# Performance work log

Hardware: AMD Instinct MI355X
Metric: run time of the kernel (lower is better)

## Reference

```python
import jax, jax.numpy as jnp
import numpy as np

N = 100000
IN_CH, HID_CH, OUT_CH = 128, 128, 64
E = 1600000


def gcn_layer(x, W, b, src, dst, num_nodes):
    """PyG GCNConv: add self-loops, symmetric deg^-1/2 normalization,
    x' = D^-1/2 (A+I) D^-1/2 (x W) + b."""
    # degrees including self-loops (deg = 1 + in-degree with unit edge weights)
    ones = jnp.ones(dst.shape[0], dtype=x.dtype)
    deg = jnp.ones(num_nodes, dtype=x.dtype).at[dst].add(ones)
    dinv = jax.lax.rsqrt(deg)
    h = x @ W  # [N, out_dim] -- transform before propagate (PyG order)
    # neighbor messages
    norm = dinv[src] * dinv[dst]                      # [E]
    msg = h[src] * norm[:, None]                      # [E, out_dim] (traffic-bound)
    agg = jax.ops.segment_sum(msg, dst, num_segments=num_nodes)
    # self-loop contribution: norm_ii = dinv[i]^2
    agg = agg + h * (dinv * dinv)[:, None]
    return agg + b


def setup_inputs() -> dict:
    key = jax.random.key(0)
    ks = jax.random.split(key, 7)
    x = jax.random.normal(ks[0], (N, IN_CH), dtype=jnp.float32)
    edge_index = jax.random.randint(ks[1], (2, E), 0, N, dtype=jnp.int64)
    # Glorot-style init like PyG GCNConv
    W1 = jax.random.normal(ks[2], (IN_CH, HID_CH), dtype=jnp.float32) * (1.0 / np.sqrt(IN_CH))
    b1 = jnp.zeros((HID_CH,), dtype=jnp.float32)
    W2 = jax.random.normal(ks[3], (HID_CH, OUT_CH), dtype=jnp.float32) * (1.0 / np.sqrt(HID_CH))
    b2 = jnp.zeros((OUT_CH,), dtype=jnp.float32)
    return {"x": x, "edge_index": edge_index, "W1": W1, "b1": b1, "W2": W2, "b2": b2}


def reference(x, edge_index, W1, b1, W2, b2):
    src, dst = edge_index[0], edge_index[1]
    h = gcn_layer(x, W1, b1, src, dst, N)
    h = jax.nn.relu(h)  # dropout is identity in eval mode
    out = gcn_layer(h, W2, b2, src, dst, N)
    return out
```

## Files before the change

kernel.cpp:

```cpp
#include <hip/hip_runtime.h>
#include <hip/hip_fp16.h>

#define NNODES 100000
#define NEDGES 1600000
#define IN_C   128
#define HID_C  128
#define OUT_C  64

#define CAP     64
#define OVF_MAX 4096

#define BUCKET_SHIFT 7
#define BUCKET_NODES 128
#define NB ((NNODES + BUCKET_NODES - 1) / BUCKET_NODES)
#define BCAP 3072
#define BCNT_STRIDE 16
#define EB 4096
#define NBLK_A ((NEDGES + EB - 1) / EB)
#define GB ((NNODES + 63) / 64)

typedef __attribute__((ext_vector_type(8))) _Float16 half8;
typedef __attribute__((ext_vector_type(4))) _Float16 half4;
typedef __attribute__((ext_vector_type(4))) float floatx4;

__device__ __forceinline__ long long load_idx(const void* p, long long i, int is64) {
  return is64 ? ((const long long*)p)[i] : (long long)((const int*)p)[i];
}

__global__ void prep_kernel(const void* eidx, int* flag, int* bcnt,
                            int* ovf_cnt, int* ovfA_cnt,
                            const float* __restrict__ W1,
                            const float* __restrict__ W2,
                            _Float16* __restrict__ Wt1,
                            _Float16* __restrict__ Wt2) {
  int i = blockIdx.x * 256 + threadIdx.x;
  if (i < NB * BCNT_STRIDE) bcnt[i] = 0;
  if (i == 0) { *ovf_cnt = 0; *ovfA_cnt = 0; }
  if (blockIdx.x == 0 && threadIdx.x < 64) {
    const unsigned* w = (const unsigned*)eidx;
    unsigned v = w[2 * threadIdx.x + 1];
    unsigned long long bad = __ballot(v != 0u);
    if (threadIdx.x == 0) *flag = (bad == 0ull) ? 1 : 0;
  }
  const int stride = gridDim.x * 256;
  for (int t = i; t < IN_C * HID_C; t += stride) {
    int n = t >> 7, k = t & 127;
    Wt1[t] = (_Float16)W1[k * HID_C + n];
  }
  for (int t = i; t < HID_C * OUT_C; t += stride) {
    int n = t >> 7, k = t & 127;
    Wt2[t] = (_Float16)W2[k * OUT_C + n];
  }
}

__global__ __launch_bounds__(512) void binA_kernel(const void* __restrict__ eidx,
                                                   const int* __restrict__ flag,
                                                   int* __restrict__ bcnt,
                                                   unsigned* __restrict__ buf,
                                                   int* __restrict__ ovfA_cnt,
                                                   int2* __restrict__ ovfA) {
  __shared__ unsigned se[EB];
  __shared__ unsigned short be[EB];
  __shared__ int hist[NB];
  __shared__ int base[NB];
  __shared__ int ofs[NB];
  const int tid = threadIdx.x;
  const int e0 = blockIdx.x * EB;
  const int e1 = min(e0 + EB, NEDGES);
  const int m = e1 - e0;
  const int is64 = *flag;

  for (int b = tid; b < NB; b += 512) { hist[b] = 0; ofs[b] = 0; }
  __syncthreads();

  for (int k = tid; k < m; k += 512) {
    int e = e0 + k;
    int s = (int)load_idx(eidx, e, is64);
    int d = (int)load_idx(eidx, (long long)NEDGES + e, is64);
    int b = d >> BUCKET_SHIFT;
    se[k] = (unsigned)s | ((unsigned)(d & (BUCKET_NODES - 1)) << 17);
    be[k] = (unsigned short)b;
    atomicAdd(&hist[b], 1);
  }
  __syncthreads();

  int rot = (blockIdx.x * 131) % NB;
  for (int idx = tid; idx < NB; idx += 512) {
    int b = idx + rot;
    if (b >= NB) b -= NB;
    int h = hist[b];
    if (h > 0) base[b] = atomicAdd(&bcnt[b * BCNT_STRIDE], h);
  }
  __syncthreads();

  for (int k = tid; k < m; k += 512) {
    unsigned u = se[k];
    int b = be[k];
    int ko = atomicAdd(&ofs[b], 1);
    int slot = base[b] + ko;
    if (slot < BCAP) {
      buf[(size_t)b * BCAP + slot] = u;
    } else {
      int p = atomicAdd(ovfA_cnt, 1);
      if (p < OVF_MAX)
        ovfA[p] = make_int2((int)(u & 0x1FFFFu),
                            (b << BUCKET_SHIFT) | (int)(u >> 17));
    }
  }
}

__global__ __launch_bounds__(512) void binB_kernel(const int* __restrict__ bcnt,
                                                   const unsigned* __restrict__ buf,
                                                   const int* __restrict__ ovfA_cnt,
                                                   const int2* __restrict__ ovfA,
                                                   int* __restrict__ cnt,
                                                   float* __restrict__ dinv,
                                                   int* __restrict__ pad_csr,
                                                   int* __restrict__ ovf_cnt,
                                                   int2* __restrict__ ovf) {
  __shared__ int pad[BUCKET_NODES * CAP];
  __shared__ int lcnt[BUCKET_NODES];
  const int b = blockIdx.x;
  const int tid = threadIdx.x;
  const int node0 = b << BUCKET_SHIFT;

  if (tid < BUCKET_NODES) lcnt[tid] = 0;
  __syncthreads();

  const int n = min(bcnt[b * BCNT_STRIDE], BCAP);
  for (int k = tid; k < n; k += 512) {
    unsigned u = buf[(size_t)b * BCAP + k];
    int s = (int)(u & 0x1FFFFu);
    int dl = (int)(u >> 17);
    int slot = atomicAdd(&lcnt[dl], 1);
    if (slot < CAP) {
      pad[dl * CAP + slot] = s;
    } else {
      int p = atomicAdd(ovf_cnt, 1);
      if (p < OVF_MAX) ovf[p] = make_int2(s, node0 + dl);
    }
  }
  int na = min(*ovfA_cnt, OVF_MAX);
  for (int t = tid; t < na; t += 512) {
    int2 p = ovfA[t];
    if ((p.y >> BUCKET_SHIFT) == b) {
      int dl = p.y & (BUCKET_NODES - 1);
      int slot = atomicAdd(&lcnt[dl], 1);
      if (slot < CAP) {
        pad[dl * CAP + slot] = p.x;
      } else {
        int q = atomicAdd(ovf_cnt, 1);
        if (q < OVF_MAX) ovf[q] = make_int2(p.x, p.y);
      }
    }
  }
  __syncthreads();

  constexpr int I4PN = CAP / 4;
  for (int q = tid; q < BUCKET_NODES * I4PN; q += 512) {
    int dl = q / I4PN;
    int gn = node0 + dl;
    if (gn < NNODES) {
      int c = (q % I4PN) * 4;
      *(int4*)&pad_csr[(size_t)gn * CAP + c] = *(const int4*)&pad[dl * CAP + c];
    }
  }
  if (tid < BUCKET_NODES && node0 + tid < NNODES) {
    int c = lcnt[tid];
    cnt[node0 + tid] = c;
    dinv[node0 + tid] = rsqrtf((float)(c + 1));
  }
}

__global__ __launch_bounds__(256) void gemm1_kernel(const float* __restrict__ x,
                                                    const _Float16* __restrict__ Wt1,
                                                    const float* __restrict__ dinv,
                                                    _Float16* __restrict__ h1s) {
  constexpr int K = IN_C, N = HID_C, KP = K + 8;
  __shared__ alignas(16) _Float16 Alds[64 * KP];
  __shared__ alignas(16) _Float16 Wlds[N * KP];
  const int tid = threadIdx.x;
  const int row0 = blockIdx.x * 64;

  for (int idx = tid; idx < N * (K / 8); idx += 256) {
    int n = idx >> 4, k16 = idx & 15;
    *(int4*)&Wlds[n * KP + k16 * 8] = *(const int4*)&Wt1[n * K + k16 * 8];
  }
  constexpr int F4PR = K / 4;
  for (int idx = tid; idx < 64 * F4PR; idx += 256) {
    int lr = idx >> 5;
    int c4 = (idx & 31) * 4;
    int gr = row0 + lr;
    if (gr > NNODES - 1) gr = NNODES - 1;
    float4 v = *(const float4*)&x[(size_t)gr * K + c4];
    half4 h = {(_Float16)v.x, (_Float16)v.y, (_Float16)v.z, (_Float16)v.w};
    *(half4*)&Alds[lr * KP + c4] = h;
  }
  __syncthreads();

  const int w = tid >> 6;
  const int lane = tid & 63;
  const int g = lane >> 4;
  const int mi = lane & 15;
  constexpr int NT = N / 16;
  floatx4 acc[NT];
#pragma unroll
  for (int t = 0; t < NT; ++t) acc[t] = (floatx4){0.f, 0.f, 0.f, 0.f};
  const _Float16* arow = &Alds[(w * 16 + mi) * KP];
#pragma unroll
  for (int ks = 0; ks < K / 32; ++ks) {
    half8 a = *(const half8*)(arow + ks * 32 + g * 8);
#pragma unroll
    for (int t = 0; t < NT; ++t) {
      half8 b = *(const half8*)&Wlds[(t * 16 + mi) * KP + ks * 32 + g * 8];
      acc[t] = __builtin_amdgcn_mfma_f32_16x16x32_f16(a, b, acc[t], 0, 0, 0);
    }
  }
#pragma unroll
  for (int r = 0; r < 4; ++r) {
    int grow = row0 + w * 16 + 4 * g + r;
    if (grow < NNODES) {
      float s = dinv[grow];
      _Float16* orow = h1s + (size_t)grow * N + mi;
#pragma unroll
      for (int t = 0; t < NT; ++t) orow[t * 16] = (_Float16)(acc[t][r] * s);
    }
  }
}

__global__ __launch_bounds__(256) void gemm2_kernel(const _Float16* __restrict__ hid,
                                                    const _Float16* __restrict__ Wt2,
                                                    const float* __restrict__ dinv,
                                                    _Float16* __restrict__ h2s) {
  constexpr int K = HID_C, N = OUT_C, KP = K + 8;
  __shared__ alignas(16) _Float16 Alds[64 * KP];
  __shared__ alignas(16) _Float16 Wlds[N * KP];
  const int tid = threadIdx.x;
  const int row0 = blockIdx.x * 64;

  for (int idx = tid; idx < N * (K / 8); idx += 256) {
    int n = idx >> 4, k16 = idx & 15;
    *(int4*)&Wlds[n * KP + k16 * 8] = *(const int4*)&Wt2[n * K + k16 * 8];
  }
  for (int idx = tid; idx < 64 * (K / 8); idx += 256) {
    int lr = idx >> 4, k16 = idx & 15;
    int gr = row0 + lr;
    if (gr > NNODES - 1) gr = NNODES - 1;
    *(int4*)&Alds[lr * KP + k16 * 8] =
        *(const int4*)&hid[(size_t)gr * K + k16 * 8];
  }
  __syncthreads();

  const int w = tid >> 6;
  const int lane = tid & 63;
  const int g = lane >> 4;
  const int mi = lane & 15;
  constexpr int NT = N / 16;
  floatx4 acc[NT];
#pragma unroll
  for (int t = 0; t < NT; ++t) acc[t] = (floatx4){0.f, 0.f, 0.f, 0.f};
  const _Float16* arow = &Alds[(w * 16 + mi) * KP];
#pragma unroll
  for (int ks = 0; ks < K / 32; ++ks) {
    half8 a = *(const half8*)(arow + ks * 32 + g * 8);
#pragma unroll
    for (int t = 0; t < NT; ++t) {
      half8 b = *(const half8*)&Wlds[(t * 16 + mi) * KP + ks * 32 + g * 8];
      acc[t] = __builtin_amdgcn_mfma_f32_16x16x32_f16(a, b, acc[t], 0, 0, 0);
    }
  }
#pragma unroll
  for (int r = 0; r < 4; ++r) {
    int grow = row0 + w * 16 + 4 * g + r;
    if (grow < NNODES) {
      float s = dinv[grow];
      _Float16* orow = h2s + (size_t)grow * N + mi;
#pragma unroll
      for (int t = 0; t < NT; ++t) orow[t * 16] = (_Float16)(acc[t][r] * s);
    }
  }
}

struct F8 {
  float x0, x1, x2, x3, x4, x5, x6, x7;
};

__device__ __forceinline__ void add_h8(F8& a, const __half* p) {
  int4 r = *(const int4*)p;
  const __half2* h = (const __half2*)&r;
  float2 f0 = __half22float2(h[0]);
  float2 f1 = __half22float2(h[1]);
  float2 f2 = __half22float2(h[2]);
  float2 f3 = __half22float2(h[3]);
  a.x0 += f0.x; a.x1 += f0.y; a.x2 += f1.x; a.x3 += f1.y;
  a.x4 += f2.x; a.x5 += f2.y; a.x6 += f3.x; a.x7 += f3.y;
}

__global__ __launch_bounds__(256) void gather1_kernel(
    const int* __restrict__ cnt, const int* __restrict__ pad_csr,
    const float* __restrict__ dinv, const __half* __restrict__ Hs1,
    const float* __restrict__ b1, const int* __restrict__ ovf_cnt,
    const int2* __restrict__ ovf, _Float16* __restrict__ hidden) {
  constexpr int C = HID_C;
  const int half = blockIdx.x & 1;
  const int tile = blockIdx.x >> 1;
  const int il = threadIdx.x >> 2;
  const int c16 = half * 64 + (threadIdx.x & 3) * 16;
  const int i = tile * 64 + il;
  if (i >= NNODES) return;

  const float di = dinv[i];
  const int deg = cnt[i];
  const int beg = i * CAP;
  const int end = beg + min(deg, CAP);
  const int* __restrict__ lst = pad_csr;
  const __half* __restrict__ Hb = Hs1 + c16;

  F8 a0l = {}, a0h = {}, a1l = {}, a1h = {};
  {
    const __half* p = Hb + (size_t)i * C;
    add_h8(a0l, p);
    add_h8(a0h, p + 8);
  }
  int j = beg;
  for (; j + 8 <= end; j += 8) {
    int4 sa = *(const int4*)&lst[j];
    int4 sb = *(const int4*)&lst[j + 4];
    const __half* p0 = Hb + (size_t)sa.x * C;
    const __half* p1 = Hb + (size_t)sa.y * C;
    const __half* p2 = Hb + (size_t)sa.z * C;
    const __half* p3 = Hb + (size_t)sa.w * C;
    add_h8(a0l, p0); add_h8(a0h, p0 + 8);
    add_h8(a1l, p1); add_h8(a1h, p1 + 8);
    add_h8(a0l, p2); add_h8(a0h, p2 + 8);
    add_h8(a1l, p3); add_h8(a1h, p3 + 8);
    const __half* p4 = Hb + (size_t)sb.x * C;
    const __half* p5 = Hb + (size_t)sb.y * C;
    const __half* p6 = Hb + (size_t)sb.z * C;
    const __half* p7 = Hb + (size_t)sb.w * C;
    add_h8(a0l, p4); add_h8(a0h, p4 + 8);
    add_h8(a1l, p5); add_h8(a1h, p5 + 8);
    add_h8(a0l, p6); add_h8(a0h, p6 + 8);
    add_h8(a1l, p7); add_h8(a1h, p7 + 8);
  }
  for (; j + 2 <= end; j += 2) {
    const __half* p0 = Hb + (size_t)lst[j] * C;
    const __half* p1 = Hb + (size_t)lst[j + 1] * C;
    add_h8(a0l, p0); add_h8(a0h, p0 + 8);
    add_h8(a1l, p1); add_h8(a1h, p1 + 8);
  }
  if (j < end) {
    const __half* p0 = Hb + (size_t)lst[j] * C;
    add_h8(a0l, p0); add_h8(a0h, p0 + 8);
  }
  if (deg > CAP) {
    int nv = min(*ovf_cnt, OVF_MAX);
    for (int t = 0; t < nv; ++t) {
      int2 p = ovf[t];
      if (p.y == i) {
        const __half* q = Hb + (size_t)p.x * C;
        add_h8(a0l, q); add_h8(a0h, q + 8);
      }
    }
  }

  float4 bb0 = *(const float4*)&b1[c16];
  float4 bb1 = *(const float4*)&b1[c16 + 4];
  float4 bb2 = *(const float4*)&b1[c16 + 8];
  float4 bb3 = *(const float4*)&b1[c16 + 12];
  float o0 = fmaf(a0l.x0 + a1l.x0, di, bb0.x);
  float o1 = fmaf(a0l.x1 + a1l.x1, di, bb0.y);
  float o2 = fmaf(a0l.x2 + a1l.x2, di, bb0.z);
  float o3 = fmaf(a0l.x3 + a1l.x3, di, bb0.w);
  float o4 = fmaf(a0l.x4 + a1l.x4, di, bb1.x);
  float o5 = fmaf(a0l.x5 + a1l.x5, di, bb1.y);
  float o6 = fmaf(a0l.x6 + a1l.x6, di, bb1.z);
  float o7 = fmaf(a0l.x7 + a1l.x7, di, bb1.w);
  float o8 = fmaf(a0h.x0 + a1h.x0, di, bb2.x);
  float o9 = fmaf(a0h.x1 + a1h.x1, di, bb2.y);
  float o10 = fmaf(a0h.x2 + a1h.x2, di, bb2.z);
  float o11 = fmaf(a0h.x3 + a1h.x3, di, bb2.w);
  float o12 = fmaf(a0h.x4 + a1h.x4, di, bb3.x);
  float o13 = fmaf(a0h.x5 + a1h.x5, di, bb3.y);
  float o14 = fmaf(a0h.x6 + a1h.x6, di, bb3.z);
  float o15 = fmaf(a0h.x7 + a1h.x7, di, bb3.w);
  o0 = o0 > 0.f ? o0 : 0.f;   o1 = o1 > 0.f ? o1 : 0.f;
  o2 = o2 > 0.f ? o2 : 0.f;   o3 = o3 > 0.f ? o3 : 0.f;
  o4 = o4 > 0.f ? o4 : 0.f;   o5 = o5 > 0.f ? o5 : 0.f;
  o6 = o6 > 0.f ? o6 : 0.f;   o7 = o7 > 0.f ? o7 : 0.f;
  o8 = o8 > 0.f ? o8 : 0.f;   o9 = o9 > 0.f ? o9 : 0.f;
  o10 = o10 > 0.f ? o10 : 0.f; o11 = o11 > 0.f ? o11 : 0.f;
  o12 = o12 > 0.f ? o12 : 0.f; o13 = o13 > 0.f ? o13 : 0.f;
  o14 = o14 > 0.f ? o14 : 0.f; o15 = o15 > 0.f ? o15 : 0.f;

  _Float16* Out = hidden + (size_t)i * C + c16;
  half8 hv0 = {(_Float16)o0, (_Float16)o1, (_Float16)o2, (_Float16)o3,
               (_Float16)o4, (_Float16)o5, (_Float16)o6, (_Float16)o7};
  half8 hv1 = {(_Float16)o8, (_Float16)o9, (_Float16)o10, (_Float16)o11,
               (_Float16)o12, (_Float16)o13, (_Float16)o14, (_Float16)o15};
  *(half8*)Out = hv0;
  *(half8*)(Out + 8) = hv1;
}

__global__ __launch_bounds__(256) void gather2_kernel(
    const int* __restrict__ cnt, const int* __restrict__ pad_csr,
    const float* __restrict__ dinv, const __half* __restrict__ Hs2,
    const float* __restrict__ b2, const int* __restrict__ ovf_cnt,
    const int2* __restrict__ ovf, float* __restrict__ Out) {
  constexpr int C = OUT_C;
  const int half = blockIdx.x & 1;
  const int tile = blockIdx.x >> 1;
  const int il = threadIdx.x >> 1;
  const int c16 = half * 32 + (threadIdx.x & 1) * 16;
  const int i = tile * 128 + il;
  if (i >= NNODES) return;

  const float di = dinv[i];
  const int deg = cnt[i];
  const int beg = i * CAP;
  const int end = beg + min(deg, CAP);
  const int* __restrict__ lst = pad_csr;
  const __half* __restrict__ Hb = Hs2 + c16;

  F8 a0l = {}, a0h = {}, a1l = {}, a1h = {};
  {
    const __half* p = Hb + (size_t)i * C;
    add_h8(a0l, p);
    add_h8(a0h, p + 8);
  }
  int j = beg;
  for (; j + 8 <= end; j += 8) {
    int4 sa = *(const int4*)&lst[j];
    int4 sb = *(const int4*)&lst[j + 4];
    const __half* p0 = Hb + (size_t)sa.x * C;
    const __half* p1 = Hb + (size_t)sa.y * C;
    const __half* p2 = Hb + (size_t)sa.z * C;
    const __half* p3 = Hb + (size_t)sa.w * C;
    add_h8(a0l, p0); add_h8(a0h, p0 + 8);
    add_h8(a1l, p1); add_h8(a1h, p1 + 8);
    add_h8(a0l, p2); add_h8(a0h, p2 + 8);
    add_h8(a1l, p3); add_h8(a1h, p3 + 8);
    const __half* p4 = Hb + (size_t)sb.x * C;
    const __half* p5 = Hb + (size_t)sb.y * C;
    const __half* p6 = Hb + (size_t)sb.z * C;
    const __half* p7 = Hb + (size_t)sb.w * C;
    add_h8(a0l, p4); add_h8(a0h, p4 + 8);
    add_h8(a1l, p5); add_h8(a1h, p5 + 8);
    add_h8(a0l, p6); add_h8(a0h, p6 + 8);
    add_h8(a1l, p7); add_h8(a1h, p7 + 8);
  }
  for (; j + 2 <= end; j += 2) {
    const __half* p0 = Hb + (size_t)lst[j] * C;
    const __half* p1 = Hb + (size_t)lst[j + 1] * C;
    add_h8(a0l, p0); add_h8(a0h, p0 + 8);
    add_h8(a1l, p1); add_h8(a1h, p1 + 8);
  }
  if (j < end) {
    const __half* p0 = Hb + (size_t)lst[j] * C;
    add_h8(a0l, p0); add_h8(a0h, p0 + 8);
  }
  if (deg > CAP) {
    int nv = min(*ovf_cnt, OVF_MAX);
    for (int t = 0; t < nv; ++t) {
      int2 p = ovf[t];
      if (p.y == i) {
        const __half* q = Hb + (size_t)p.x * C;
        add_h8(a0l, q); add_h8(a0h, q + 8);
      }
    }
  }

  float4 bb0 = *(const float4*)&b2[c16];
  float4 bb1 = *(const float4*)&b2[c16 + 4];
  float4 bb2 = *(const float4*)&b2[c16 + 8];
  float4 bb3 = *(const float4*)&b2[c16 + 12];
  float* O = Out + (size_t)i * C + c16;
  *(float4*)O = make_float4(fmaf(a0l.x0 + a1l.x0, di, bb0.x),
                            fmaf(a0l.x1 + a1l.x1, di, bb0.y),
                            fmaf(a0l.x2 + a1l.x2, di, bb0.z),
                            fmaf(a0l.x3 + a1l.x3, di, bb0.w));
  *(float4*)(O + 4) = make_float4(fmaf(a0l.x4 + a1l.x4, di, bb1.x),
                                  fmaf(a0l.x5 + a1l.x5, di, bb1.y),
                                  fmaf(a0l.x6 + a1l.x6, di, bb1.z),
                                  fmaf(a0l.x7 + a1l.x7, di, bb1.w));
  *(float4*)(O + 8) = make_float4(fmaf(a0h.x0 + a1h.x0, di, bb2.x),
                                  fmaf(a0h.x1 + a1h.x1, di, bb2.y),
                                  fmaf(a0h.x2 + a1h.x2, di, bb2.z),
                                  fmaf(a0h.x3 + a1h.x3, di, bb2.w));
  *(float4*)(O + 12) = make_float4(fmaf(a0h.x4 + a1h.x4, di, bb3.x),
                                   fmaf(a0h.x5 + a1h.x5, di, bb3.y),
                                   fmaf(a0h.x6 + a1h.x6, di, bb3.z),
                                   fmaf(a0h.x7 + a1h.x7, di, bb3.w));
}

extern "C" void kernel_launch(void* const* d_in, const int* in_sizes, int n_in,
                              void* d_out, int out_size, void* d_ws, size_t ws_size,
                              hipStream_t stream) {
  const float* x = (const float*)d_in[0];
  const void* eidx = d_in[1];
  const float* W1 = (const float*)d_in[2];
  const float* b1 = (const float*)d_in[3];
  const float* W2 = (const float*)d_in[4];
  const float* b2 = (const float*)d_in[5];
  float* out = (float*)d_out;
  char* ws = (char*)d_ws;

  int*      flag     = (int*)(ws + 0);
  int*      ovf_cnt  = (int*)(ws + 512);
  int*      ovfA_cnt = (int*)(ws + 1024);
  int*      bcnt     = (int*)(ws + 1536);
  int*      cnt      = (int*)(ws + 52224);
  float*    dinv     = (float*)(ws + 452608);
  int2*     ovf      = (int2*)(ws + 852992);
  int2*     ovfA     = (int2*)(ws + 885760);
  _Float16* Wt1      = (_Float16*)(ws + 918528);
  _Float16* Wt2      = (_Float16*)(ws + 951296);
  unsigned* buf      = (unsigned*)(ws + 968192);
  int*      pad_csr  = (int*)(ws + 10577920);
  _Float16* h1s      = (_Float16*)(ws + 36178432);
  _Float16* hidden   = (_Float16*)(ws + 61778944);
  _Float16* h2s      = h1s;

  prep_kernel<<<(NB * BCNT_STRIDE + 255) / 256, 256, 0, stream>>>(
      eidx, flag, bcnt, ovf_cnt, ovfA_cnt, W1, W2, Wt1, Wt2);
  binA_kernel<<<NBLK_A, 512, 0, stream>>>(eidx, flag, bcnt, buf, ovfA_cnt, ovfA);
  binB_kernel<<<NB, 512, 0, stream>>>(bcnt, buf, ovfA_cnt, ovfA, cnt, dinv,
                                      pad_csr, ovf_cnt, ovf);
  gemm1_kernel<<<GB, 256, 0, stream>>>(x, Wt1, dinv, h1s);
  gather1_kernel<<<2 * GB, 256, 0, stream>>>(cnt, pad_csr, dinv,
                                             (const __half*)h1s, b1,
                                             ovf_cnt, ovf, hidden);
  gemm2_kernel<<<GB, 256, 0, stream>>>(hidden, Wt2, dinv, h2s);
  gather2_kernel<<<2 * ((NNODES + 127) / 128), 256, 0, stream>>>(
      cnt, pad_csr, dinv, (const __half*)h2s, b2, ovf_cnt, ovf, out);
}
```

Baseline: 293.0 us.

## Fuse edge binning with first GEMM, apply source norm in gather, halve CSR cap

The first GEMM is merged into the edge-binning kernel as extra blocks, so it no longer depends on degree normalisation. It now writes an unscaled h1 and overlaps with binning. The layer-1 gather multiplies each neighbour row by dinv[src] itself, which adds one scattered dinv load per edge. The padded CSR capacity drops from 64 to 32, which shrinks pad_csr traffic and workspace but relies on the overflow list for high-degree nodes. The gather index mapping is also simplified to a flat thread-per-16-channel layout.

```diff
diff --git a/kernel.cpp b/kernel.cpp
--- a/kernel.cpp
+++ b/kernel.cpp
@@ -7,7 +7,7 @@
 #define HID_C  128
 #define OUT_C  64
 
-#define CAP     64
+#define CAP     32
 #define OVF_MAX 4096
 
 #define BUCKET_SHIFT 7
@@ -53,58 +53,111 @@
   }
 }
 
-__global__ __launch_bounds__(512) void binA_kernel(const void* __restrict__ eidx,
-                                                   const int* __restrict__ flag,
-                                                   int* __restrict__ bcnt,
-                                                   unsigned* __restrict__ buf,
-                                                   int* __restrict__ ovfA_cnt,
-                                                   int2* __restrict__ ovfA) {
-  __shared__ unsigned se[EB];
-  __shared__ unsigned short be[EB];
-  __shared__ int hist[NB];
-  __shared__ int base[NB];
-  __shared__ int ofs[NB];
+__global__ __launch_bounds__(256) void binA_gemm1_kernel(
+    const void* __restrict__ eidx, const int* __restrict__ flag,
+    int* __restrict__ bcnt, unsigned* __restrict__ buf,
+    int* __restrict__ ovfA_cnt, int2* __restrict__ ovfA,
+    const float* __restrict__ x, const _Float16* __restrict__ Wt1,
+    _Float16* __restrict__ h1u) {
+  __shared__ alignas(16) char smem[52224];
   const int tid = threadIdx.x;
-  const int e0 = blockIdx.x * EB;
-  const int e1 = min(e0 + EB, NEDGES);
-  const int m = e1 - e0;
-  const int is64 = *flag;
-
-  for (int b = tid; b < NB; b += 512) { hist[b] = 0; ofs[b] = 0; }
-  __syncthreads();
-
-  for (int k = tid; k < m; k += 512) {
-    int e = e0 + k;
-    int s = (int)load_idx(eidx, e, is64);
-    int d = (int)load_idx(eidx, (long long)NEDGES + e, is64);
-    int b = d >> BUCKET_SHIFT;
-    se[k] = (unsigned)s | ((unsigned)(d & (BUCKET_NODES - 1)) << 17);
-    be[k] = (unsigned short)b;
-    atomicAdd(&hist[b], 1);
-  }
-  __syncthreads();
-
-  int rot = (blockIdx.x * 131) % NB;
-  for (int idx = tid; idx < NB; idx += 512) {
-    int b = idx + rot;
-    if (b >= NB) b -= NB;
-    int h = hist[b];
-    if (h > 0) base[b] = atomicAdd(&bcnt[b * BCNT_STRIDE], h);
-  }
-  __syncthreads();
-
-  for (int k = tid; k < m; k += 512) {
-    unsigned u = se[k];
-    int b = be[k];
-    int ko = atomicAdd(&ofs[b], 1);
-    int slot = base[b] + ko;
-    if (slot < BCAP) {
-      buf[(size_t)b * BCAP + slot] = u;
-    } else {
-      int p = atomicAdd(ovfA_cnt, 1);
-      if (p < OVF_MAX)
-        ovfA[p] = make_int2((int)(u & 0x1FFFFu),
-                            (b << BUCKET_SHIFT) | (int)(u >> 17));
+
+  if (blockIdx.x < NBLK_A) {
+    unsigned* se = (unsigned*)smem;
+    unsigned short* be = (unsigned short*)(smem + 16384);
+    int* hist = (int*)(smem + 24576);
+    int* base = (int*)(smem + 27712);
+    int* ofs  = (int*)(smem + 30848);
+    const int e0 = blockIdx.x * EB;
+    const int e1 = min(e0 + EB, NEDGES);
+    const int m = e1 - e0;
+    const int is64 = *flag;
+
+    for (int b = tid; b < NB; b += 256) { hist[b] = 0; ofs[b] = 0; }
+    __syncthreads();
+
+    for (int k = tid; k < m; k += 256) {
+      int e = e0 + k;
+      int s = (int)load_idx(eidx, e, is64);
+      int d = (int)load_idx(eidx, (long long)NEDGES + e, is64);
+      int b = d >> BUCKET_SHIFT;
+      se[k] = (unsigned)s | ((unsigned)(d & (BUCKET_NODES - 1)) << 17);
+      be[k] = (unsigned short)b;
+      atomicAdd(&hist[b], 1);
+    }
+    __syncthreads();
+
+    int rot = (blockIdx.x * 131) % NB;
+    for (int idx = tid; idx < NB; idx += 256) {
+      int b = idx + rot;
+      if (b >= NB) b -= NB;
+      int h = hist[b];
+      if (h > 0) base[b] = atomicAdd(&bcnt[b * BCNT_STRIDE], h);
+    }
+    __syncthreads();
+
+    for (int k = tid; k < m; k += 256) {
+      unsigned u = se[k];
+      int b = be[k];
+      int ko = atomicAdd(&ofs[b], 1);
+      int slot = base[b] + ko;
+      if (slot < BCAP) {
+        buf[(size_t)b * BCAP + slot] = u;
+      } else {
+        int p = atomicAdd(ovfA_cnt, 1);
+        if (p < OVF_MAX)
+          ovfA[p] = make_int2((int)(u & 0x1FFFFu),
+                              (b << BUCKET_SHIFT) | (int)(u >> 17));
+      }
+    }
+  } else {
+    constexpr int K = IN_C, N = HID_C, KP = K + 8;
+    _Float16* Alds = (_Float16*)smem;
+    _Float16* Wlds = (_Float16*)(smem + 17408);
+    const int row0 = (blockIdx.x - NBLK_A) * 64;
+
+    for (int idx = tid; idx < N * (K / 8); idx += 256) {
+      int n = idx >> 4, k16 = idx & 15;
+      *(int4*)&Wlds[n * KP + k16 * 8] = *(const int4*)&Wt1[n * K + k16 * 8];
+    }
+    constexpr int F4PR = K / 4;
+    for (int idx = tid; idx < 64 * F4PR; idx += 256) {
+      int lr = idx >> 5;
+      int c4 = (idx & 31) * 4;
+      int gr = row0 + lr;
+      if (gr > NNODES - 1) gr = NNODES - 1;
+      float4 v = *(const float4*)&x[(size_t)gr * K + c4];
+      half4 h = {(_Float16)v.x, (_Float16)v.y, (_Float16)v.z, (_Float16)v.w};
+      *(half4*)&Alds[lr * KP + c4] = h;
+    }
+    __syncthreads();
+
+    const int w = tid >> 6;
+    const int lane = tid & 63;
+    const int g = lane >> 4;
+    const int mi = lane & 15;
+    constexpr int NT = N / 16;
+    floatx4 acc[NT];
+#pragma unroll
+    for (int t = 0; t < NT; ++t) acc[t] = (floatx4){0.f, 0.f, 0.f, 0.f};
+    const _Float16* arow = &Alds[(w * 16 + mi) * KP];
+#pragma unroll
+    for (int ks = 0; ks < K / 32; ++ks) {
+      half8 a = *(const half8*)(arow + ks * 32 + g * 8);
+#pragma unroll
+      for (int t = 0; t < NT; ++t) {
+        half8 b = *(const half8*)&Wlds[(t * 16 + mi) * KP + ks * 32 + g * 8];
+        acc[t] = __builtin_amdgcn_mfma_f32_16x16x32_f16(a, b, acc[t], 0, 0, 0);
+      }
+    }
+#pragma unroll
+    for (int r = 0; r < 4; ++r) {
+      int grow = row0 + w * 16 + 4 * g + r;
+      if (grow < NNODES) {
+        _Float16* orow = h1u + (size_t)grow * N + mi;
+#pragma unroll
+        for (int t = 0; t < NT; ++t) orow[t * 16] = (_Float16)acc[t][r];
+      }
     }
   }
 }
@@ -172,60 +225,137 @@
   }
 }
 
-__global__ __launch_bounds__(256) void gemm1_kernel(const float* __restrict__ x,
-                                                    const _Float16* __restrict__ Wt1,
-                                                    const float* __restrict__ dinv,
-                                                    _Float16* __restrict__ h1s) {
-  constexpr int K = IN_C, N = HID_C, KP = K + 8;
-  __shared__ alignas(16) _Float16 Alds[64 * KP];
-  __shared__ alignas(16) _Float16 Wlds[N * KP];
-  const int tid = threadIdx.x;
-  const int row0 = blockIdx.x * 64;
-
-  for (int idx = tid; idx < N * (K / 8); idx += 256) {
-    int n = idx >> 4, k16 = idx & 15;
-    *(int4*)&Wlds[n * KP + k16 * 8] = *(const int4*)&Wt1[n * K + k16 * 8];
-  }
-  constexpr int F4PR = K / 4;
-  for (int idx = tid; idx < 64 * F4PR; idx += 256) {
-    int lr = idx >> 5;
-    int c4 = (idx & 31) * 4;
-    int gr = row0 + lr;
-    if (gr > NNODES - 1) gr = NNODES - 1;
-    float4 v = *(const float4*)&x[(size_t)gr * K + c4];
-    half4 h = {(_Float16)v.x, (_Float16)v.y, (_Float16)v.z, (_Float16)v.w};
-    *(half4*)&Alds[lr * KP + c4] = h;
-  }
-  __syncthreads();
-
-  const int w = tid >> 6;
-  const int lane = tid & 63;
-  const int g = lane >> 4;
-  const int mi = lane & 15;
-  constexpr int NT = N / 16;
-  floatx4 acc[NT];
-#pragma unroll
-  for (int t = 0; t < NT; ++t) acc[t] = (floatx4){0.f, 0.f, 0.f, 0.f};
-  const _Float16* arow = &Alds[(w * 16 + mi) * KP];
-#pragma unroll
-  for (int ks = 0; ks < K / 32; ++ks) {
-    half8 a = *(const half8*)(arow + ks * 32 + g * 8);
-#pragma unroll
-    for (int t = 0; t < NT; ++t) {
-      half8 b = *(const half8*)&Wlds[(t * 16 + mi) * KP + ks * 32 + g * 8];
-      acc[t] = __builtin_amdgcn_mfma_f32_16x16x32_f16(a, b, acc[t], 0, 0, 0);
-    }
-  }
-#pragma unroll
-  for (int r = 0; r < 4; ++r) {
-    int grow = row0 + w * 16 + 4 * g + r;
-    if (grow < NNODES) {
-      float s = dinv[grow];
-      _Float16* orow = h1s + (size_t)grow * N + mi;
-#pragma unroll
-      for (int t = 0; t < NT; ++t) orow[t * 16] = (_Float16)(acc[t][r] * s);
-    }
-  }
+struct F8 {
+  float x0, x1, x2, x3, x4, x5, x6, x7;
+};
+
+__device__ __forceinline__ void add_h8(F8& a, const __half* p) {
+  int4 r = *(const int4*)p;
+  const __half2* h = (const __half2*)&r;
+  float2 f0 = __half22float2(h[0]);
+  float2 f1 = __half22float2(h[1]);
+  float2 f2 = __half22float2(h[2]);
+  float2 f3 = __half22float2(h[3]);
+  a.x0 += f0.x; a.x1 += f0.y; a.x2 += f1.x; a.x3 += f1.y;
+  a.x4 += f2.x; a.x5 += f2.y; a.x6 += f3.x; a.x7 += f3.y;
+}
+
+__device__ __forceinline__ void add_h8s(F8& a, const __half* p, float s) {
+  int4 r = *(const int4*)p;
+  const __half2* h = (const __half2*)&r;
+  float2 f0 = __half22float2(h[0]);
+  float2 f1 = __half22float2(h[1]);
+  float2 f2 = __half22float2(h[2]);
+  float2 f3 = __half22float2(h[3]);
+  a.x0 = fmaf(s, f0.x, a.x0); a.x1 = fmaf(s, f0.y, a.x1);
+  a.x2 = fmaf(s, f1.x, a.x2); a.x3 = fmaf(s, f1.y, a.x3);
+  a.x4 = fmaf(s, f2.x, a.x4); a.x5 = fmaf(s, f2.y, a.x5);
+  a.x6 = fmaf(s, f3.x, a.x6); a.x7 = fmaf(s, f3.y, a.x7);
+}
+
+__global__ __launch_bounds__(256) void gather1d_kernel(
+    const int* __restrict__ cnt, const int* __restrict__ pad_csr,
+    const float* __restrict__ dinv, const __half* __restrict__ H,
+    const float* __restrict__ b1, const int* __restrict__ ovf_cnt,
+    const int2* __restrict__ ovf, _Float16* __restrict__ hidden) {
+  constexpr int C = HID_C;
+  constexpr int TPN = C / 16;
+  int gid = blockIdx.x * 256 + threadIdx.x;
+  int i = gid / TPN;
+  int c16 = (gid % TPN) * 16;
+  if (i >= NNODES) return;
+
+  const float di = dinv[i];
+  const int deg = cnt[i];
+  const int beg = i * CAP;
+  const int end = beg + min(deg, CAP);
+  const int* __restrict__ lst = pad_csr;
+  const __half* __restrict__ Hb = H + c16;
+
+  F8 a0l = {}, a0h = {}, a1l = {}, a1h = {};
+  {
+    const __half* p = Hb + (size_t)i * C;
+    add_h8s(a0l, p, di);
+    add_h8s(a0h, p + 8, di);
+  }
+  int j = beg;
+  for (; j + 8 <= end; j += 8) {
+    int4 sa = *(const int4*)&lst[j];
+    int4 sb = *(const int4*)&lst[j + 4];
+    float d0 = dinv[sa.x], d1 = dinv[sa.y], d2 = dinv[sa.z], d3 = dinv[sa.w];
+    float d4 = dinv[sb.x], d5 = dinv[sb.y], d6 = dinv[sb.z], d7 = dinv[sb.w];
+    const __half* p0 = Hb + (size_t)sa.x * C;
+    const __half* p1 = Hb + (size_t)sa.y * C;
+    const __half* p2 = Hb + (size_t)sa.z * C;
+    const __half* p3 = Hb + (size_t)sa.w * C;
+    add_h8s(a0l, p0, d0); add_h8s(a0h, p0 + 8, d0);
+    add_h8s(a1l, p1, d1); add_h8s(a1h, p1 + 8, d1);
+    add_h8s(a0l, p2, d2); add_h8s(a0h, p2 + 8, d2);
+    add_h8s(a1l, p3, d3); add_h8s(a1h, p3 + 8, d3);
+    const __half* p4 = Hb + (size_t)sb.x * C;
+    const __half* p5 = Hb + (size_t)sb.y * C;
+    const __half* p6 = Hb + (size_t)sb.z * C;
+    const __half* p7 = Hb + (size_t)sb.w * C;
+    add_h8s(a0l, p4, d4); add_h8s(a0h, p4 + 8, d4);
+    add_h8s(a1l, p5, d5); add_h8s(a1h, p5 + 8, d5);
+    add_h8s(a0l, p6, d6); add_h8s(a0h, p6 + 8, d6);
+    add_h8s(a1l, p7, d7); add_h8s(a1h, p7 + 8, d7);
+  }
+  for (; j < end; ++j) {
+    int s = lst[j];
+    float ds = dinv[s];
+    const __half* p0 = Hb + (size_t)s * C;
+    add_h8s(a0l, p0, ds); add_h8s(a0h, p0 + 8, ds);
+  }
+  if (deg > CAP) {
+    int nv = min(*ovf_cnt, OVF_MAX);
+    for (int t = 0; t < nv; ++t) {
+      int2 p = ovf[t];
+      if (p.y == i) {
+        float ds = dinv[p.x];
+        const __half* q = Hb + (size_t)p.x * C;
+        add_h8s(a0l, q, ds); add_h8s(a0h, q + 8, ds);
+      }
+    }
+  }
+
+  float s0 = a0l.x0 + a1l.x0, s1 = a0l.x1 + a1l.x1;
+  float s2 = a0l.x2 + a1l.x2, s3 = a0l.x3 + a1l.x3;
+  float s4 = a0l.x4 + a1l.x4, s5 = a0l.x5 + a1l.x5;
+  float s6 = a0l.x6 + a1l.x6, s7 = a0l.x7 + a1l.x7;
+  float s8 = a0h.x0 + a1h.x0, s9 = a0h.x1 + a1h.x1;
+  float s10 = a0h.x2 + a1h.x2, s11 = a0h.x3 + a1h.x3;
+  float s12 = a0h.x4 + a1h.x4, s13 = a0h.x5 + a1h.x5;
+  float s14 = a0h.x6 + a1h.x6, s15 = a0h.x7 + a1h.x7;
+
+  float4 bb0 = *(const float4*)&b1[c16];
+  float4 bb1 = *(const float4*)&b1[c16 + 4];
+  float4 bb2 = *(const float4*)&b1[c16 + 8];
+  float4 bb3 = *(const float4*)&b1[c16 + 12];
+  float o0 = fmaf(s0, di, bb0.x),  o1 = fmaf(s1, di, bb0.y);
+  float o2 = fmaf(s2, di, bb0.z),  o3 = fmaf(s3, di, bb0.w);
+  float o4 = fmaf(s4, di, bb1.x),  o5 = fmaf(s5, di, bb1.y);
+  float o6 = fmaf(s6, di, bb1.z),  o7 = fmaf(s7, di, bb1.w);
+  float o8 = fmaf(s8, di, bb2.x),  o9 = fmaf(s9, di, bb2.y);
+  float o10 = fmaf(s10, di, bb2.z), o11 = fmaf(s11, di, bb2.w);
+  float o12 = fmaf(s12, di, bb3.x), o13 = fmaf(s13, di, bb3.y);
+  float o14 = fmaf(s14, di, bb3.z), o15 = fmaf(s15, di, bb3.w);
+  o0 = o0 > 0.f ? o0 : 0.f;   o1 = o1 > 0.f ? o1 : 0.f;
+  o2 = o2 > 0.f ? o2 : 0.f;   o3 = o3 > 0.f ? o3 : 0.f;
+  o4 = o4 > 0.f ? o4 : 0.f;   o5 = o5 > 0.f ? o5 : 0.f;
+  o6 = o6 > 0.f ? o6 : 0.f;   o7 = o7 > 0.f ? o7 : 0.f;
+  o8 = o8 > 0.f ? o8 : 0.f;   o9 = o9 > 0.f ? o9 : 0.f;
+  o10 = o10 > 0.f ? o10 : 0.f; o11 = o11 > 0.f ? o11 : 0.f;
+  o12 = o12 > 0.f ? o12 : 0.f; o13 = o13 > 0.f ? o13 : 0.f;
+  o14 = o14 > 0.f ? o14 : 0.f; o15 = o15 > 0.f ? o15 : 0.f;
+
+  _Float16* Out = hidden + (size_t)i * C + c16;
+  half8 hv0 = {(_Float16)o0, (_Float16)o1, (_Float16)o2, (_Float16)o3,
+               (_Float16)o4, (_Float16)o5, (_Float16)o6, (_Float16)o7};
+  half8 hv1 = {(_Float16)o8, (_Float16)o9, (_Float16)o10, (_Float16)o11,
+               (_Float16)o12, (_Float16)o13, (_Float16)o14, (_Float16)o15};
+  *(half8*)Out = hv0;
+  *(half8*)(Out + 8) = hv1;
 }
 
 __global__ __launch_bounds__(256) void gemm2_kernel(const _Float16* __restrict__ hid,
@@ -281,138 +411,16 @@
   }
 }
 
-struct F8 {
-  float x0, x1, x2, x3, x4, x5, x6, x7;
-};
-
-__device__ __forceinline__ void add_h8(F8& a, const __half* p) {
-  int4 r = *(const int4*)p;
-  const __half2* h = (const __half2*)&r;
-  float2 f0 = __half22float2(h[0]);
-  float2 f1 = __half22float2(h[1]);
-  float2 f2 = __half22float2(h[2]);
-  float2 f3 = __half22float2(h[3]);
-  a.x0 += f0.x; a.x1 += f0.y; a.x2 += f1.x; a.x3 += f1.y;
-  a.x4 += f2.x; a.x5 += f2.y; a.x6 += f3.x; a.x7 += f3.y;
-}
-
-__global__ __launch_bounds__(256) void gather1_kernel(
-    const int* __restrict__ cnt, const int* __restrict__ pad_csr,
-    const float* __restrict__ dinv, const __half* __restrict__ Hs1,
-    const float* __restrict__ b1, const int* __restrict__ ovf_cnt,
-    const int2* __restrict__ ovf, _Float16* __restrict__ hidden) {
-  constexpr int C = HID_C;
-  const int half = blockIdx.x & 1;
-  const int tile = blockIdx.x >> 1;
-  const int il = threadIdx.x >> 2;
-  const int c16 = half * 64 + (threadIdx.x & 3) * 16;
-  const int i = tile * 64 + il;
-  if (i >= NNODES) return;
-
-  const float di = dinv[i];
-  const int deg = cnt[i];
-  const int beg = i * CAP;
-  const int end = beg + min(deg, CAP);
-  const int* __restrict__ lst = pad_csr;
-  const __half* __restrict__ Hb = Hs1 + c16;
-
-  F8 a0l = {}, a0h = {}, a1l = {}, a1h = {};
-  {
-    const __half* p = Hb + (size_t)i * C;
-    add_h8(a0l, p);
-    add_h8(a0h, p + 8);
-  }
-  int j = beg;
-  for (; j + 8 <= end; j += 8) {
-    int4 sa = *(const int4*)&lst[j];
-    int4 sb = *(const int4*)&lst[j + 4];
-    const __half* p0 = Hb + (size_t)sa.x * C;
-    const __half* p1 = Hb + (size_t)sa.y * C;
-    const __half* p2 = Hb + (size_t)sa.z * C;
-    const __half* p3 = Hb + (size_t)sa.w * C;
-    add_h8(a0l, p0); add_h8(a0h, p0 + 8);
-    add_h8(a1l, p1); add_h8(a1h, p1 + 8);
-    add_h8(a0l, p2); add_h8(a0h, p2 + 8);
-    add_h8(a1l, p3); add_h8(a1h, p3 + 8);
-    const __half* p4 = Hb + (size_t)sb.x * C;
-    const __half* p5 = Hb + (size_t)sb.y * C;
-    const __half* p6 = Hb + (size_t)sb.z * C;
-    const __half* p7 = Hb + (size_t)sb.w * C;
-    add_h8(a0l, p4); add_h8(a0h, p4 + 8);
-    add_h8(a1l, p5); add_h8(a1h, p5 + 8);
-    add_h8(a0l, p6); add_h8(a0h, p6 + 8);
-    add_h8(a1l, p7); add_h8(a1h, p7 + 8);
-  }
-  for (; j + 2 <= end; j += 2) {
-    const __half* p0 = Hb + (size_t)lst[j] * C;
-    const __half* p1 = Hb + (size_t)lst[j + 1] * C;
-    add_h8(a0l, p0); add_h8(a0h, p0 + 8);
-    add_h8(a1l, p1); add_h8(a1h, p1 + 8);
-  }
-  if (j < end) {
-    const __half* p0 = Hb + (size_t)lst[j] * C;
-    add_h8(a0l, p0); add_h8(a0h, p0 + 8);
-  }
-  if (deg > CAP) {
-    int nv = min(*ovf_cnt, OVF_MAX);
-    for (int t = 0; t < nv; ++t) {
-      int2 p = ovf[t];
-      if (p.y == i) {
-        const __half* q = Hb + (size_t)p.x * C;
-        add_h8(a0l, q); add_h8(a0h, q + 8);
-      }
-    }
-  }
-
-  float4 bb0 = *(const float4*)&b1[c16];
-  float4 bb1 = *(const float4*)&b1[c16 + 4];
-  float4 bb2 = *(const float4*)&b1[c16 + 8];
-  float4 bb3 = *(const float4*)&b1[c16 + 12];
-  float o0 = fmaf(a0l.x0 + a1l.x0, di, bb0.x);
-  float o1 = fmaf(a0l.x1 + a1l.x1, di, bb0.y);
-  float o2 = fmaf(a0l.x2 + a1l.x2, di, bb0.z);
-  float o3 = fmaf(a0l.x3 + a1l.x3, di, bb0.w);
-  float o4 = fmaf(a0l.x4 + a1l.x4, di, bb1.x);
-  float o5 = fmaf(a0l.x5 + a1l.x5, di, bb1.y);
-  float o6 = fmaf(a0l.x6 + a1l.x6, di, bb1.z);
-  float o7 = fmaf(a0l.x7 + a1l.x7, di, bb1.w);
-  float o8 = fmaf(a0h.x0 + a1h.x0, di, bb2.x);
-  float o9 = fmaf(a0h.x1 + a1h.x1, di, bb2.y);
-  float o10 = fmaf(a0h.x2 + a1h.x2, di, bb2.z);
-  float o11 = fmaf(a0h.x3 + a1h.x3, di, bb2.w);
-  float o12 = fmaf(a0h.x4 + a1h.x4, di, bb3.x);
-  float o13 = fmaf(a0h.x5 + a1h.x5, di, bb3.y);
-  float o14 = fmaf(a0h.x6 + a1h.x6, di, bb3.z);
-  float o15 = fmaf(a0h.x7 + a1h.x7, di, bb3.w);
-  o0 = o0 > 0.f ? o0 : 0.f;   o1 = o1 > 0.f ? o1 : 0.f;
-  o2 = o2 > 0.f ? o2 : 0.f;   o3 = o3 > 0.f ? o3 : 0.f;
-  o4 = o4 > 0.f ? o4 : 0.f;   o5 = o5 > 0.f ? o5 : 0.f;
-  o6 = o6 > 0.f ? o6 : 0.f;   o7 = o7 > 0.f ? o7 : 0.f;
-  o8 = o8 > 0.f ? o8 : 0.f;   o9 = o9 > 0.f ? o9 : 0.f;
-  o10 = o10 > 0.f ? o10 : 0.f; o11 = o11 > 0.f ? o11 : 0.f;
-  o12 = o12 > 0.f ? o12 : 0.f; o13 = o13 > 0.f ? o13 : 0.f;
-  o14 = o14 > 0.f ? o14 : 0.f; o15 = o15 > 0.f ? o15 : 0.f;
-
-  _Float16* Out = hidden + (size_t)i * C + c16;
-  half8 hv0 = {(_Float16)o0, (_Float16)o1, (_Float16)o2, (_Float16)o3,
-               (_Float16)o4, (_Float16)o5, (_Float16)o6, (_Float16)o7};
-  half8 hv1 = {(_Float16)o8, (_Float16)o9, (_Float16)o10, (_Float16)o11,
-               (_Float16)o12, (_Float16)o13, (_Float16)o14, (_Float16)o15};
-  *(half8*)Out = hv0;
-  *(half8*)(Out + 8) = hv1;
-}
-
 __global__ __launch_bounds__(256) void gather2_kernel(
     const int* __restrict__ cnt, const int* __restrict__ pad_csr,
     const float* __restrict__ dinv, const __half* __restrict__ Hs2,
     const float* __restrict__ b2, const int* __restrict__ ovf_cnt,
     const int2* __restrict__ ovf, float* __restrict__ Out) {
   constexpr int C = OUT_C;
-  const int half = blockIdx.x & 1;
-  const int tile = blockIdx.x >> 1;
-  const int il = threadIdx.x >> 1;
-  const int c16 = half * 32 + (threadIdx.x & 1) * 16;
-  const int i = tile * 128 + il;
+  constexpr int TPN = C / 16;
+  int gid = blockIdx.x * 256 + threadIdx.x;
+  int i = gid / TPN;
+  int c16 = (gid % TPN) * 16;
   if (i >= NNODES) return;
 
   const float di = dinv[i];
@@ -517,20 +525,19 @@
   _Float16* Wt2      = (_Float16*)(ws + 951296);
   unsigned* buf      = (unsigned*)(ws + 968192);
   int*      pad_csr  = (int*)(ws + 10577920);
-  _Float16* h1s      = (_Float16*)(ws + 36178432);
-  _Float16* hidden   = (_Float16*)(ws + 61778944);
-  _Float16* h2s      = h1s;
+  _Float16* h1u      = (_Float16*)(ws + 23378432);
+  _Float16* hidden   = (_Float16*)(ws + 48978944);
+  _Float16* h2s      = h1u;
 
   prep_kernel<<<(NB * BCNT_STRIDE + 255) / 256, 256, 0, stream>>>(
       eidx, flag, bcnt, ovf_cnt, ovfA_cnt, W1, W2, Wt1, Wt2);
-  binA_kernel<<<NBLK_A, 512, 0, stream>>>(eidx, flag, bcnt, buf, ovfA_cnt, ovfA);
+  binA_gemm1_kernel<<<NBLK_A + GB, 256, 0, stream>>>(eidx, flag, bcnt, buf,
+                                                     ovfA_cnt, ovfA, x, Wt1, h1u);
   binB_kernel<<<NB, 512, 0, stream>>>(bcnt, buf, ovfA_cnt, ovfA, cnt, dinv,
                                       pad_csr, ovf_cnt, ovf);
-  gemm1_kernel<<<GB, 256, 0, stream>>>(x, Wt1, dinv, h1s);
-  gather1_kernel<<<2 * GB, 256, 0, stream>>>(cnt, pad_csr, dinv,
-                                             (const __half*)h1s, b1,
-                                             ovf_cnt, ovf, hidden);
+  gather1d_kernel<<<(NNODES * (HID_C / 16) + 255) / 256, 256, 0, stream>>>(
+      cnt, pad_csr, dinv, (const __half*)h1u, b1, ovf_cnt, ovf, hidden);
   gemm2_kernel<<<GB, 256, 0, stream>>>(hidden, Wt2, dinv, h2s);
-  gather2_kernel<<<2 * ((NNODES + 127) / 128), 256, 0, stream>>>(
+  gather2_kernel<<<(NNODES * (OUT_C / 16) + 255) / 256, 256, 0, stream>>>(
       cnt, pad_csr, dinv, (const __half*)h2s, b2, ovf_cnt, ovf, out);
 }
```

Measured after the change: 271.8 us. -7.3%, faster.
